# Optimization experiments

Hardware: AMD Instinct MI355X
Metric: run time of the kernel (lower is better)

The kernel has to match this reference:

```python
import jax, jax.numpy as jnp
from jax import lax
import numpy as np

B, L, N_NODES, EMB, TDIM, H, NCLS = 512, 200, 100000, 128, 10, 256, 2
IN = TDIM + EMB  # 138


def setup_inputs() -> dict:
    key = jax.random.key(0)
    ks = jax.random.split(key, 16)
    x = jax.random.randint(ks[0], (B, L, 2), 0, N_NODES, dtype=jnp.int64)
    s = 0.05
    inp = {
        'x': x,
        'emb_table': jax.random.normal(ks[1], (N_NODES, EMB), jnp.float32) * s,
        'ts_W': jnp.ones((1, TDIM), jnp.float32),
        'w_ih_f': jax.random.normal(ks[2], (4 * H, IN), jnp.float32) * s,
        'w_hh_f': jax.random.normal(ks[3], (4 * H, H), jnp.float32) * s,
        'b_ih_f': jax.random.normal(ks[4], (4 * H,), jnp.float32) * s,
        'b_hh_f': jax.random.normal(ks[5], (4 * H,), jnp.float32) * s,
        'w_ih_b': jax.random.normal(ks[6], (4 * H, IN), jnp.float32) * s,
        'w_hh_b': jax.random.normal(ks[7], (4 * H, H), jnp.float32) * s,
        'b_ih_b': jax.random.normal(ks[8], (4 * H,), jnp.float32) * s,
        'b_hh_b': jax.random.normal(ks[9], (4 * H,), jnp.float32) * s,
        'fc_W': jax.random.normal(ks[10], (NCLS, 2 * H), jnp.float32) * s,
        'fc_b': jax.random.normal(ks[11], (NCLS,), jnp.float32) * s,
    }
    return inp


def _lstm_dir(x_seq, w_ih, w_hh, b_ih, b_hh, reverse):
    # x_seq: [B, L, F]; PyTorch gate order i, f, g, o
    bsz = x_seq.shape[0]
    h_dim = w_hh.shape[1]
    xg = jnp.einsum('blf,gf->blg', x_seq, w_ih) + b_ih + b_hh  # [B, L, 4H]
    xs = jnp.swapaxes(xg, 0, 1)  # [L, B, 4H]
    if reverse:
        xs = xs[::-1]

    def step(carry, xg_t):
        h, c = carry
        g = xg_t + h @ w_hh.T
        i, f, gg, o = jnp.split(g, 4, axis=-1)
        c = jax.nn.sigmoid(f) * c + jax.nn.sigmoid(i) * jnp.tanh(gg)
        h = jax.nn.sigmoid(o) * jnp.tanh(c)
        return (h, c), h

    z = jnp.zeros((bsz, h_dim), x_seq.dtype)
    _, hs = lax.scan(step, (z, z), xs)
    hs = jnp.swapaxes(hs, 0, 1)  # [B, L, H]
    if reverse:
        hs = hs[:, ::-1]
    return hs


def reference(x, emb_table, ts_W, w_ih_f, w_hh_f, b_ih_f, b_hh_f,
              w_ih_b, w_hh_b, b_ih_b, b_hh_b, fc_W, fc_b):
    # timestamp embedding: [B, L, 1] @ [1, 10] -> [B, L, 10]
    t = x[:, :, 0:1].astype(jnp.float32)
    t_emb = t @ ts_W
    # F.normalize(p=2, dim=1): L2-normalize over the sequence axis
    norm = jnp.sqrt(jnp.sum(t_emb * t_emb, axis=1, keepdims=True))
    t_emb = t_emb / jnp.maximum(norm, 1e-12)

    # vectorized node-embedding gather; id == -1 -> zero vector
    ids = x[:, :, 1]
    gathered = emb_table[jnp.clip(ids, 0, None)]  # [B, L, 128]
    l_emb = jnp.where((ids >= 0)[..., None], gathered, jnp.zeros((), gathered.dtype))

    embedding = jnp.concatenate([t_emb, l_emb], axis=2)  # [B, L, 138]

    h_f = _lstm_dir(embedding, w_ih_f, w_hh_f, b_ih_f, b_hh_f, reverse=False)
    h_b = _lstm_dir(embedding, w_ih_b, w_hh_b, b_ih_b, b_hh_b, reverse=True)
    out = jnp.concatenate([h_f, h_b], axis=-1)  # [B, L, 2H]

    return out[:, -1, :] @ fc_W.T + fc_b  # [B, num_classes]
```

## Files before the change

### kernel.cpp

```cpp
#include <hip/hip_runtime.h>
#include <stdint.h>


typedef unsigned short u16;
typedef __bf16 bf16x8 __attribute__((ext_vector_type(8)));
typedef float  f32x4  __attribute__((ext_vector_type(4)));
typedef int    i32x4v __attribute__((ext_vector_type(4)));
typedef int    i32x8v __attribute__((ext_vector_type(8)));

#define B_    512
#define L_    200
#define EMB_  128
#define TDIM_ 10
#define IN_   138
#define INP_  160
#define H_    256
#define G4_   1024
#define T_    200
#define DS_   (1.0f/1024.0f)
#define LOG2E 1.4426950408889634f
#define EXP2(x) __builtin_amdgcn_exp2f(x)

static __device__ __forceinline__ float bf2f(u16 u) {
  union { uint32_t i; float f; } v; v.i = ((uint32_t)u) << 16; return v.f;
}
static __device__ __forceinline__ u16 f2bf(float f) {
  __bf16 h = (__bf16)f; return __builtin_bit_cast(u16, h);
}
static __device__ __forceinline__ float bflo(uint32_t u) {
  return __builtin_bit_cast(float, (uint32_t)(u << 16));
}
static __device__ __forceinline__ float bfhi(uint32_t u) {
  return __builtin_bit_cast(float, (uint32_t)(u & 0xffff0000u));
}
static __device__ __forceinline__ float sigf(float x) {
  return __builtin_amdgcn_rcpf(1.0f + EXP2(-x * LOG2E));
}
static __device__ __forceinline__ float tanh_(float x) {
  x = fminf(fmaxf(x, -15.f), 15.f);
  float e = EXP2(2.0f * LOG2E * x);
  return (e - 1.0f) * __builtin_amdgcn_rcpf(e + 1.0f);
}
static __device__ __forceinline__ f32x4 mfma16(bf16x8 a, bf16x8 b, f32x4 c) {
  return __builtin_amdgcn_mfma_f32_16x16x32_bf16(a, b, c, 0, 0, 0);
}
static __device__ __forceinline__ f32x4 vzero4() {
  f32x4 v; v[0] = 0.f; v[1] = 0.f; v[2] = 0.f; v[3] = 0.f; return v;
}

__global__ void k_norm(const int* __restrict__ x, float* __restrict__ s) {
  int b = blockIdx.x;
  int tid = threadIdx.x;
  float v = 0.f;
  if (tid < L_) {
    float t = (float)x[(b * L_ + tid) * 2];
    v = t * t;
  }
  #pragma unroll
  for (int o = 32; o; o >>= 1) v += __shfl_down(v, o);
  __shared__ float p[4];
  if ((tid & 63) == 0) p[tid >> 6] = v;
  __syncthreads();
  if (tid == 0) s[b] = p[0] + p[1] + p[2] + p[3];
}

__global__ void k_prep_mx(const float* __restrict__ whh, int* __restrict__ wf8) {
  int idx = blockIdx.x * blockDim.x + threadIdx.x;
  int d = idx & 7;
  int lane = (idx >> 3) & 63;
  int fs = idx >> 9;
  int kp2 = fs & 1, tt = (fs >> 1) & 7, w = fs >> 4;
  int mm = lane & 15, q = lane >> 4;
  int g = (w + 8 * tt) * 16 + mm;
  int k = kp2 * 128 + q * 32 + d * 4;
  const float* src = whh + g * 256 + k;
  int v = __builtin_amdgcn_cvt_pk_fp8_f32(src[0] * 64.f, src[1] * 64.f, 0, false);
  v     = __builtin_amdgcn_cvt_pk_fp8_f32(src[2] * 64.f, src[3] * 64.f, v, true);
  wf8[idx] = v;
}

__global__ void k_feat(const int* __restrict__ x, const float* __restrict__ emb,
                       const float* __restrict__ tsW, const float* __restrict__ s,
                       u16* __restrict__ feat) {
  int idx = blockIdx.x * blockDim.x + threadIdx.x;
  if (idx >= B_ * L_ * INP_) return;
  int c = idx % INP_;
  int row = idx / INP_;
  int b = row / L_;
  float v = 0.f;
  if (c < TDIM_) {
    float t = (float)x[row * 2 + 0];
    float wd = tsW[c];
    float den = fmaxf(fabsf(wd) * sqrtf(s[b]), 1e-12f);
    v = t * wd / den;
  } else if (c < IN_) {
    int id = x[row * 2 + 1];
    int idc = id < 0 ? 0 : id;
    float e = emb[(long)idc * EMB_ + (c - TDIM_)];
    v = (id >= 0) ? e : 0.f;
  }
  feat[idx] = f2bf(v);
}

__global__ __launch_bounds__(512) void k_xg(
    const u16* __restrict__ feat, const float* __restrict__ wih,
    const float* __restrict__ bih, const float* __restrict__ bhh,
    u16* __restrict__ xg) {
  __shared__ u16 Bs[256 * 176];
  const int nt = blockIdx.x;
  const int mt = blockIdx.y;
  const int tid = threadIdx.x;
  const int w = tid >> 6, lane = tid & 63;
  const int q = lane >> 4, nm = lane & 15;
  for (int i2 = tid; i2 < 256 * 88; i2 += 512) {
    int gl = i2 / 88, f2 = (i2 % 88) * 2;
    int pk = 0;
    if (f2 < IN_) {
      float2 v = *(const float2*)(wih + (long)(nt * 256 + gl) * IN_ + f2);
      pk = (int)f2bf(v.x) | ((int)f2bf(v.y) << 16);
    }
    *(int*)&Bs[gl * 176 + f2] = pk;
  }
  float bias[16];
  #pragma unroll
  for (int nu = 0; nu < 16; ++nu) {
    int g = nt * 256 + nu * 16 + nm;
    bias[nu] = bih[g] + bhh[g];
  }
  __syncthreads();
  f32x4 acc[16];
  #pragma unroll
  for (int nu = 0; nu < 16; ++nu) acc[nu] = vzero4();
  const u16* arow = feat + (long)(mt * 128 + w * 16) * INP_;
  #pragma unroll
  for (int kp = 0; kp < 5; ++kp) {
    bf16x8 a = *(const bf16x8*)(arow + (nm * INP_ + kp * 32 + q * 8));
    #pragma unroll
    for (int nu = 0; nu < 16; ++nu) {
      bf16x8 bb = *(const bf16x8*)&Bs[(nu * 16 + nm) * 176 + kp * 32 + q * 8];
      acc[nu] = mfma16(a, bb, acc[nu]);
    }
  }
  __syncthreads();
  u16* Os = Bs;
  #pragma unroll
  for (int nu = 0; nu < 16; ++nu) {
    #pragma unroll
    for (int r = 0; r < 4; ++r) {
      int row = w * 16 + 4 * q + r;
      Os[row * 264 + nu * 16 + nm] = f2bf((acc[nu][r] + bias[nu]) * 1024.f);
    }
  }
  __syncthreads();
  #pragma unroll
  for (int it = 0; it < 8; ++it) {
    int flat = it * 512 + tid;
    int row = flat >> 5, c = flat & 31;
    uint4 v = *(const uint4*)&Os[row * 264 + c * 8];
    *(uint4*)&xg[(long)(mt * 128 + row) * G4_ + nt * 256 + c * 8] = v;
  }
}

#define MX2(accv, A0, A1, B0, B1) \
  asm volatile("v_mfma_f32_16x16x128_f8f6f4 %0, %1, %3, %0\n\t" \
               "v_mfma_f32_16x16x128_f8f6f4 %0, %2, %4, %0" \
               : "+v"(accv) : "v"(A0), "v"(A1), "v"(B0), "v"(B1));
#define AINIT(i) \
  f32x4 acc##i; acc##i[0] = bflo(pf##i.x); acc##i[1] = bfhi(pf##i.x); \
  acc##i[2] = bflo(pf##i.y); acc##i[3] = bfhi(pf##i.y);
#define PFL(i) pf##i = *(const uint2*)(xn + ((w + 8 * (i)) * 16 + 4 * q));
#define ALDS(f) __builtin_shufflevector(ldsX[(w * 8 + (f)) * 64 + lane], \
                                        ldsY[(w * 8 + (f)) * 64 + lane], \
                                        0, 1, 2, 3, 4, 5, 6, 7)
#define EPI(jj, aI, aF, aG, aO, cs) { \
  f32x4 hv; \
  _Pragma("unroll") \
  for (int r = 0; r < 4; ++r) { \
    float si = __builtin_amdgcn_rcpf(1.f + EXP2(aI[r] * c_sig)); \
    float sf = __builtin_amdgcn_rcpf(1.f + EXP2(aF[r] * c_sig)); \
    float so = __builtin_amdgcn_rcpf(1.f + EXP2(aO[r] * c_sig)); \
    float tg = 1.f - 2.f * __builtin_amdgcn_rcpf(1.f + EXP2(aG[r] * c_tg)); \
    float c = sf * cs[r] + si * tg; \
    float tc = 1.f - 2.f * __builtin_amdgcn_rcpf(1.f + EXP2(c * c_tc)); \
    cs[r] = c; hv[r] = so * tc; \
  } \
  int pk = __builtin_amdgcn_cvt_pk_fp8_f32(hv[0] * 16.f, hv[1] * 16.f, 0, false); \
  pk     = __builtin_amdgcn_cvt_pk_fp8_f32(hv[2] * 16.f, hv[3] * 16.f, pk, true); \
  hw[nn * 68 + 4 * w + 32 * (jj) + q] = pk; \
  if (t == T_ - 1) *(f32x4*)&hf[(long)b * H_ + 16 * w + 128 * (jj) + 4 * q] = hv; }

__global__ __launch_bounds__(512, 2) void k_lstm_f(
    const int* __restrict__ wf8, const u16* __restrict__ xg,
    float* __restrict__ hf) {
  __shared__ i32x4v ldsX[64 * 64];
  __shared__ i32x4v ldsY[64 * 64];
  __shared__ int hls[2][16 * 68];
  const int tid = threadIdx.x;
  const int w = tid >> 6;
  const int lane = tid & 63;
  const int q = lane >> 4;
  const int nn = lane & 15;
  const int b = blockIdx.x * 16 + nn;
  const float c_sig = -DS_ * LOG2E;
  const float c_tg  = 2.f * DS_ * LOG2E;
  const float c_tc  = 2.f * LOG2E;

#define WREG(fi) (*(const i32x8v*)(wf8 + (long)((w * 16 + (fi)) * 64 + lane) * 8))
  i32x8v W40 = WREG(8),  W41 = WREG(9),  W50 = WREG(10), W51 = WREG(11);
  i32x8v W60 = WREG(12), W61 = WREG(13), W70 = WREG(14), W71 = WREG(15);
  #pragma unroll
  for (int f = 0; f < 8; ++f) {
    i32x8v v = WREG(f);
    ldsX[(w * 8 + f) * 64 + lane] = __builtin_shufflevector(v, v, 0, 1, 2, 3);
    ldsY[(w * 8 + f) * 64 + lane] = __builtin_shufflevector(v, v, 4, 5, 6, 7);
  }
  for (int i = tid; i < 16 * 68; i += 512) hls[0][i] = 0;

  const u16* xgb = xg + (long)b * (L_ * G4_);
  uint2 pf0, pf1, pf2, pf3, pf4, pf5, pf6, pf7;
  {
    const u16* xn = xgb;
    PFL(0) PFL(1) PFL(2) PFL(3) PFL(4) PFL(5) PFL(6) PFL(7)
  }
  f32x4 cst0 = vzero4(), cst1 = vzero4();
  __syncthreads();

  #pragma unroll 1
  for (int t = 0; t < T_; ++t) {
    AINIT(0) AINIT(1) AINIT(2) AINIT(3) AINIT(4) AINIT(5) AINIT(6) AINIT(7)
    {
      const u16* xn = xgb + (long)(t + 1 < T_ ? t + 1 : t) * G4_;
      PFL(0) PFL(1) PFL(2) PFL(3) PFL(4) PFL(5) PFL(6) PFL(7)
    }
    const int* hr = hls[t & 1];
    i32x8v B0 = __builtin_shufflevector(
        *(const i32x4v*)&hr[nn * 68 + q * 8],
        *(const i32x4v*)&hr[nn * 68 + q * 8 + 4], 0, 1, 2, 3, 4, 5, 6, 7);
    i32x8v B1 = __builtin_shufflevector(
        *(const i32x4v*)&hr[nn * 68 + 32 + q * 8],
        *(const i32x4v*)&hr[nn * 68 + 32 + q * 8 + 4], 0, 1, 2, 3, 4, 5, 6, 7);
    {
      i32x8v A0, A1;
      A0 = ALDS(0); A1 = ALDS(1); MX2(acc0, A0, A1, B0, B1);
      A0 = ALDS(2); A1 = ALDS(3); MX2(acc1, A0, A1, B0, B1);
      A0 = ALDS(4); A1 = ALDS(5); MX2(acc2, A0, A1, B0, B1);
      A0 = ALDS(6); A1 = ALDS(7); MX2(acc3, A0, A1, B0, B1);
    }
    MX2(acc4, W40, W41, B0, B1);
    MX2(acc5, W50, W51, B0, B1);
    MX2(acc6, W60, W61, B0, B1);
    MX2(acc7, W70, W71, B0, B1);
    asm volatile("s_nop 7\n\ts_nop 7"
                 : "+v"(acc4), "+v"(acc5), "+v"(acc6), "+v"(acc7));
    int* hw = hls[1 - (t & 1)];
    EPI(0, acc0, acc2, acc4, acc6, cst0)
    EPI(1, acc1, acc3, acc5, acc7, cst1)
    __asm__ volatile("" ::: "memory");
    __builtin_amdgcn_s_waitcnt(0xc07f);
    __builtin_amdgcn_s_barrier();
    __asm__ volatile("" ::: "memory");
  }
}

__global__ __launch_bounds__(256) void k_bwd(
    const u16* __restrict__ feat, const float* __restrict__ wih,
    const float* __restrict__ bih, const float* __restrict__ bhh,
    float* __restrict__ hb) {
  const int b0 = blockIdx.x * 8;
  const int tid = threadIdx.x;
  __shared__ float fv[8][IN_];
  for (int i = tid; i < 8 * IN_; i += 256) {
    int r = i / IN_, c = i % IN_;
    fv[r][c] = bf2f(feat[((long)(b0 + r) * L_ + (L_ - 1)) * INP_ + c]);
  }
  __syncthreads();
  float gi[8], gg[8], go[8];
  float bi_ = bih[tid] + bhh[tid];
  float bg_ = bih[2 * H_ + tid] + bhh[2 * H_ + tid];
  float bo_ = bih[3 * H_ + tid] + bhh[3 * H_ + tid];
  #pragma unroll
  for (int r = 0; r < 8; ++r) { gi[r] = bi_; gg[r] = bg_; go[r] = bo_; }
  const float* wi_ = wih + (long)tid * IN_;
  const float* wg_ = wih + (long)(2 * H_ + tid) * IN_;
  const float* wo_ = wih + (long)(3 * H_ + tid) * IN_;
  for (int f = 0; f < IN_; ++f) {
    float a = wi_[f], gc = wg_[f], oc = wo_[f];
    #pragma unroll
    for (int r = 0; r < 8; ++r) {
      float x = fv[r][f];
      gi[r] += a * x;
      gg[r] += gc * x;
      go[r] += oc * x;
    }
  }
  #pragma unroll
  for (int r = 0; r < 8; ++r) {
    float c = sigf(gi[r]) * tanh_(gg[r]);
    hb[(long)(b0 + r) * H_ + tid] = sigf(go[r]) * tanh_(c);
  }
}

__global__ void k_fc(const float* __restrict__ hf, const float* __restrict__ hb,
                     const float* __restrict__ fcw, const float* __restrict__ fcb,
                     float* __restrict__ out) {
  int b = blockIdx.x;
  int lane = threadIdx.x;
  float p0 = 0.f, p1 = 0.f;
  #pragma unroll
  for (int k = lane; k < 2 * H_; k += 64) {
    float v = (k < H_) ? hf[b * H_ + k] : hb[b * H_ + (k - H_)];
    p0 += v * fcw[k];
    p1 += v * fcw[2 * H_ + k];
  }
  #pragma unroll
  for (int o = 32; o; o >>= 1) {
    p0 += __shfl_down(p0, o);
    p1 += __shfl_down(p1, o);
  }
  if (lane == 0) {
    out[b * 2 + 0] = p0 + fcb[0];
    out[b * 2 + 1] = p1 + fcb[1];
  }
}

extern "C" void kernel_launch(void* const* d_in, const int* in_sizes, int n_in,
                              void* d_out, int out_size, void* d_ws, size_t ws_size,
                              hipStream_t stream) {
  const int*   x    = (const int*)  d_in[0];
  const float* emb  = (const float*)d_in[1];
  const float* tsW  = (const float*)d_in[2];
  const float* wihf = (const float*)d_in[3];
  const float* whhf = (const float*)d_in[4];
  const float* bihf = (const float*)d_in[5];
  const float* bhhf = (const float*)d_in[6];
  const float* wihb = (const float*)d_in[7];
  const float* bihb = (const float*)d_in[9];
  const float* bhhb = (const float*)d_in[10];
  const float* fcw  = (const float*)d_in[11];
  const float* fcb  = (const float*)d_in[12];
  float* out = (float*)d_out;

  char* ws = (char*)d_ws;
  float* s    = (float*)(ws);
  int*   wf8  = (int*)  (ws + 2048);
  u16*   feat = (u16*)  (ws + 264192);
  u16*   xg   = (u16*)  (ws + 33032192);
  float* hf   = (float*)(ws + 242747392);
  float* hb   = (float*)(ws + 243271680);

  k_norm   <<<dim3(512),     dim3(256), 0, stream>>>(x, s);
  k_prep_mx<<<dim3(256),     dim3(256), 0, stream>>>(whhf, wf8);
  k_feat   <<<dim3(64000),   dim3(256), 0, stream>>>(x, emb, tsW, s, feat);
  k_xg     <<<dim3(4, 800),  dim3(512), 0, stream>>>(feat, wihf, bihf, bhhf, xg);
  k_lstm_f <<<dim3(32),      dim3(512), 0, stream>>>(wf8, xg, hf);
  k_bwd    <<<dim3(64),      dim3(256), 0, stream>>>(feat, wihb, bihb, bhhb, hb);
  k_fc     <<<dim3(512),     dim3(64),  0, stream>>>(hf, hb, fcw, fcb, out);
}
```

Before: 804.3 us.

## Keep all recurrent weights in AGPRs, interleave MFMA with epilogue, double k_xg tile

The LSTM forward kernel now keeps all 16 fp8 weight fragments of W_hh in registers and feeds them to the MFMA as AGPR operands, dropping the LDS staging of half the weights and the per-step LDS reads. The MFMAs for the second half are interleaved with the gate epilogue so matrix and transcendental work overlap. The epilogue is rewritten to use fewer reciprocals per row, with exponent clamping. The xg GEMM kernel processes 256 rows per block instead of 128, reusing the LDS weight tile across twice the rows, with occupancy hinted at 2 blocks per CU. This raises register pressure and risks spills.

After: 798.8 us. About the same (-0.7%).

```diff
diff --git a/kernel.cpp b/kernel.cpp
--- a/kernel.cpp
+++ b/kernel.cpp
@@ -102,7 +102,7 @@
   feat[idx] = f2bf(v);
 }
 
-__global__ __launch_bounds__(512) void k_xg(
+__global__ __launch_bounds__(512, 2) void k_xg(
     const u16* __restrict__ feat, const float* __restrict__ wih,
     const float* __restrict__ bih, const float* __restrict__ bhh,
     u16* __restrict__ xg) {
@@ -128,72 +128,76 @@
     bias[nu] = bih[g] + bhh[g];
   }
   __syncthreads();
-  f32x4 acc[16];
-  #pragma unroll
-  for (int nu = 0; nu < 16; ++nu) acc[nu] = vzero4();
-  const u16* arow = feat + (long)(mt * 128 + w * 16) * INP_;
+  f32x4 acc[2][16];
+  #pragma unroll
+  for (int m = 0; m < 2; ++m)
+    #pragma unroll
+    for (int nu = 0; nu < 16; ++nu) acc[m][nu] = vzero4();
+  const u16* arow = feat + (long)(mt * 256 + w * 32) * INP_;
   #pragma unroll
   for (int kp = 0; kp < 5; ++kp) {
-    bf16x8 a = *(const bf16x8*)(arow + (nm * INP_ + kp * 32 + q * 8));
+    bf16x8 a0 = *(const bf16x8*)(arow + (nm * INP_ + kp * 32 + q * 8));
+    bf16x8 a1 = *(const bf16x8*)(arow + ((16 + nm) * INP_ + kp * 32 + q * 8));
     #pragma unroll
     for (int nu = 0; nu < 16; ++nu) {
       bf16x8 bb = *(const bf16x8*)&Bs[(nu * 16 + nm) * 176 + kp * 32 + q * 8];
-      acc[nu] = mfma16(a, bb, acc[nu]);
-    }
-  }
-  __syncthreads();
+      acc[0][nu] = mfma16(a0, bb, acc[0][nu]);
+      acc[1][nu] = mfma16(a1, bb, acc[1][nu]);
+    }
+  }
   u16* Os = Bs;
   #pragma unroll
-  for (int nu = 0; nu < 16; ++nu) {
+  for (int p = 0; p < 2; ++p) {
+    __syncthreads();
+    if ((w >> 2) == p) {
+      #pragma unroll
+      for (int nu = 0; nu < 16; ++nu)
+        #pragma unroll
+        for (int m = 0; m < 2; ++m)
+          #pragma unroll
+          for (int r = 0; r < 4; ++r) {
+            int row = (w & 3) * 32 + m * 16 + 4 * q + r;
+            Os[row * 264 + nu * 16 + nm] = f2bf((acc[m][nu][r] + bias[nu]) * 1024.f);
+          }
+    }
+    __syncthreads();
     #pragma unroll
-    for (int r = 0; r < 4; ++r) {
-      int row = w * 16 + 4 * q + r;
-      Os[row * 264 + nu * 16 + nm] = f2bf((acc[nu][r] + bias[nu]) * 1024.f);
-    }
-  }
-  __syncthreads();
-  #pragma unroll
-  for (int it = 0; it < 8; ++it) {
-    int flat = it * 512 + tid;
-    int row = flat >> 5, c = flat & 31;
-    uint4 v = *(const uint4*)&Os[row * 264 + c * 8];
-    *(uint4*)&xg[(long)(mt * 128 + row) * G4_ + nt * 256 + c * 8] = v;
-  }
-}
-
-#define MX2(accv, A0, A1, B0, B1) \
+    for (int it = 0; it < 8; ++it) {
+      int flat = it * 512 + tid;
+      int row = flat >> 5, c = flat & 31;
+      uint4 v = *(const uint4*)&Os[row * 264 + c * 8];
+      *(uint4*)&xg[(long)(mt * 256 + p * 128 + row) * G4_ + nt * 256 + c * 8] = v;
+    }
+  }
+}
+
+#define MX2A(accv, A0, A1, Bx, By) \
   asm volatile("v_mfma_f32_16x16x128_f8f6f4 %0, %1, %3, %0\n\t" \
                "v_mfma_f32_16x16x128_f8f6f4 %0, %2, %4, %0" \
-               : "+v"(accv) : "v"(A0), "v"(A1), "v"(B0), "v"(B1));
+               : "+v"(accv) : "a"(A0), "a"(A1), "v"(Bx), "v"(By));
 #define AINIT(i) \
   f32x4 acc##i; acc##i[0] = bflo(pf##i.x); acc##i[1] = bfhi(pf##i.x); \
   acc##i[2] = bflo(pf##i.y); acc##i[3] = bfhi(pf##i.y);
 #define PFL(i) pf##i = *(const uint2*)(xn + ((w + 8 * (i)) * 16 + 4 * q));
-#define ALDS(f) __builtin_shufflevector(ldsX[(w * 8 + (f)) * 64 + lane], \
-                                        ldsY[(w * 8 + (f)) * 64 + lane], \
-                                        0, 1, 2, 3, 4, 5, 6, 7)
-#define EPI(jj, aI, aF, aG, aO, cs) { \
-  f32x4 hv; \
-  _Pragma("unroll") \
-  for (int r = 0; r < 4; ++r) { \
-    float si = __builtin_amdgcn_rcpf(1.f + EXP2(aI[r] * c_sig)); \
-    float sf = __builtin_amdgcn_rcpf(1.f + EXP2(aF[r] * c_sig)); \
-    float so = __builtin_amdgcn_rcpf(1.f + EXP2(aO[r] * c_sig)); \
-    float tg = 1.f - 2.f * __builtin_amdgcn_rcpf(1.f + EXP2(aG[r] * c_tg)); \
-    float c = sf * cs[r] + si * tg; \
-    float tc = 1.f - 2.f * __builtin_amdgcn_rcpf(1.f + EXP2(c * c_tc)); \
-    cs[r] = c; hv[r] = so * tc; \
-  } \
-  int pk = __builtin_amdgcn_cvt_pk_fp8_f32(hv[0] * 16.f, hv[1] * 16.f, 0, false); \
-  pk     = __builtin_amdgcn_cvt_pk_fp8_f32(hv[2] * 16.f, hv[3] * 16.f, pk, true); \
+#define EPIROW(r, cs, aI, aF, aG, aO, hv) { \
+  float ei = EXP2((aI)[r] * c_sig); \
+  float ef = EXP2((aF)[r] * c_sig); \
+  float eo = EXP2((aO)[r] * c_sig); \
+  float eg = EXP2(fminf((aG)[r] * c_tg, 126.f)); \
+  float c  = cs[r] * __builtin_amdgcn_rcpf(1.f + ef) \
+           + (eg - 1.f) * __builtin_amdgcn_rcpf((1.f + ei) * (1.f + eg)); \
+  cs[r] = c; \
+  float ec = EXP2(fminf(c * c_tc, 126.f)); \
+  (hv)[r] = (ec - 1.f) * __builtin_amdgcn_rcpf((1.f + eo) * (1.f + ec)); }
+#define HPACK(jj, hv) { \
+  int pk = __builtin_amdgcn_cvt_pk_fp8_f32((hv)[0] * 16.f, (hv)[1] * 16.f, 0, false); \
+  pk     = __builtin_amdgcn_cvt_pk_fp8_f32((hv)[2] * 16.f, (hv)[3] * 16.f, pk, true); \
   hw[nn * 68 + 4 * w + 32 * (jj) + q] = pk; \
-  if (t == T_ - 1) *(f32x4*)&hf[(long)b * H_ + 16 * w + 128 * (jj) + 4 * q] = hv; }
+  if (t == T_ - 1) *(f32x4*)&hf[(long)b * H_ + 16 * w + 128 * (jj) + 4 * q] = (hv); }
 
 __global__ __launch_bounds__(512, 2) void k_lstm_f(
     const int* __restrict__ wf8, const u16* __restrict__ xg,
     float* __restrict__ hf) {
-  __shared__ i32x4v ldsX[64 * 64];
-  __shared__ i32x4v ldsY[64 * 64];
   __shared__ int hls[2][16 * 68];
   const int tid = threadIdx.x;
   const int w = tid >> 6;
@@ -206,14 +210,10 @@
   const float c_tc  = 2.f * LOG2E;
 
 #define WREG(fi) (*(const i32x8v*)(wf8 + (long)((w * 16 + (fi)) * 64 + lane) * 8))
+  i32x8v W00 = WREG(0),  W01 = WREG(1),  W10 = WREG(2),  W11 = WREG(3);
+  i32x8v W20 = WREG(4),  W21 = WREG(5),  W30 = WREG(6),  W31 = WREG(7);
   i32x8v W40 = WREG(8),  W41 = WREG(9),  W50 = WREG(10), W51 = WREG(11);
   i32x8v W60 = WREG(12), W61 = WREG(13), W70 = WREG(14), W71 = WREG(15);
-  #pragma unroll
-  for (int f = 0; f < 8; ++f) {
-    i32x8v v = WREG(f);
-    ldsX[(w * 8 + f) * 64 + lane] = __builtin_shufflevector(v, v, 0, 1, 2, 3);
-    ldsY[(w * 8 + f) * 64 + lane] = __builtin_shufflevector(v, v, 4, 5, 6, 7);
-  }
   for (int i = tid; i < 16 * 68; i += 512) hls[0][i] = 0;
 
   const u16* xgb = xg + (long)b * (L_ * G4_);
@@ -239,22 +239,31 @@
     i32x8v B1 = __builtin_shufflevector(
         *(const i32x4v*)&hr[nn * 68 + 32 + q * 8],
         *(const i32x4v*)&hr[nn * 68 + 32 + q * 8 + 4], 0, 1, 2, 3, 4, 5, 6, 7);
-    {
-      i32x8v A0, A1;
-      A0 = ALDS(0); A1 = ALDS(1); MX2(acc0, A0, A1, B0, B1);
-      A0 = ALDS(2); A1 = ALDS(3); MX2(acc1, A0, A1, B0, B1);
-      A0 = ALDS(4); A1 = ALDS(5); MX2(acc2, A0, A1, B0, B1);
-      A0 = ALDS(6); A1 = ALDS(7); MX2(acc3, A0, A1, B0, B1);
-    }
-    MX2(acc4, W40, W41, B0, B1);
-    MX2(acc5, W50, W51, B0, B1);
-    MX2(acc6, W60, W61, B0, B1);
-    MX2(acc7, W70, W71, B0, B1);
+    MX2A(acc0, W00, W01, B0, B1);
+    MX2A(acc2, W20, W21, B0, B1);
+    MX2A(acc4, W40, W41, B0, B1);
+    MX2A(acc6, W60, W61, B0, B1);
+    MX2A(acc1, W10, W11, B0, B1);
+    MX2A(acc3, W30, W31, B0, B1);
     asm volatile("s_nop 7\n\ts_nop 7"
-                 : "+v"(acc4), "+v"(acc5), "+v"(acc6), "+v"(acc7));
+                 : "+v"(acc0), "+v"(acc2), "+v"(acc4), "+v"(acc6));
     int* hw = hls[1 - (t & 1)];
-    EPI(0, acc0, acc2, acc4, acc6, cst0)
-    EPI(1, acc1, acc3, acc5, acc7, cst1)
+    f32x4 hv0;
+    EPIROW(0, cst0, acc0, acc2, acc4, acc6, hv0)
+    MX2A(acc5, W50, W51, B0, B1);
+    EPIROW(1, cst0, acc0, acc2, acc4, acc6, hv0)
+    MX2A(acc7, W70, W71, B0, B1);
+    EPIROW(2, cst0, acc0, acc2, acc4, acc6, hv0)
+    EPIROW(3, cst0, acc0, acc2, acc4, acc6, hv0)
+    HPACK(0, hv0)
+    asm volatile("s_nop 7\n\ts_nop 7"
+                 : "+v"(acc1), "+v"(acc3), "+v"(acc5), "+v"(acc7));
+    f32x4 hv1;
+    EPIROW(0, cst1, acc1, acc3, acc5, acc7, hv1)
+    EPIROW(1, cst1, acc1, acc3, acc5, acc7, hv1)
+    EPIROW(2, cst1, acc1, acc3, acc5, acc7, hv1)
+    EPIROW(3, cst1, acc1, acc3, acc5, acc7, hv1)
+    HPACK(1, hv1)
     __asm__ volatile("" ::: "memory");
     __builtin_amdgcn_s_waitcnt(0xc07f);
     __builtin_amdgcn_s_barrier();
@@ -351,7 +360,7 @@
   k_norm   <<<dim3(512),     dim3(256), 0, stream>>>(x, s);
   k_prep_mx<<<dim3(256),     dim3(256), 0, stream>>>(whhf, wf8);
   k_feat   <<<dim3(64000),   dim3(256), 0, stream>>>(x, emb, tsW, s, feat);
-  k_xg     <<<dim3(4, 800),  dim3(512), 0, stream>>>(feat, wihf, bihf, bhhf, xg);
+  k_xg     <<<dim3(4, 400),  dim3(512), 0, stream>>>(feat, wihf, bihf, bhhf, xg);
   k_lstm_f <<<dim3(32),      dim3(512), 0, stream>>>(wf8, xg, hf);
   k_bwd    <<<dim3(64),      dim3(256), 0, stream>>>(feat, wihb, bihb, bhhb, hb);
   k_fc     <<<dim3(512),     dim3(64),  0, stream>>>(hf, hb, fcw, fcb, out);
```
